# Kernel tuning notes

Hardware: AMD Instinct MI355X
Metric: run time of the kernel (lower is better)

Reference implementation:

```python
import jax, jax.numpy as jnp
import numpy as np

B, N, C, H = 4, 2048, 768, 12
D = C // H  # head_dim = 64

def setup_inputs() -> dict:
    key = jax.random.key(0)
    ks = jax.random.split(key, 6)
    s = 0.02
    return {
        "img_tokens": jax.random.normal(ks[0], (B, N, C), jnp.float32),
        "ln_gamma": jnp.ones((C,), jnp.float32),
        "ln_beta": jnp.zeros((C,), jnp.float32),
        "w_qkv": jax.random.normal(ks[1], (C, 3 * C), jnp.float32) * s,
        "w_out": jax.random.normal(ks[2], (C, C), jnp.float32) * s,
        "b_out": jnp.zeros((C,), jnp.float32),
    }

def reference(img_tokens, ln_gamma, ln_beta, w_qkv, w_out, b_out):
    x = img_tokens
    # LayerNorm over channel dim
    mu = jnp.mean(x, axis=-1, keepdims=True)
    var = jnp.var(x, axis=-1, keepdims=True)
    xn = (x - mu) * jax.lax.rsqrt(var + 1e-5) * ln_gamma + ln_beta
    qkv = xn @ w_qkv                      # [B, N, 3C]
    q, k, v = jnp.split(qkv, 3, axis=-1)
    def heads(t):                          # [B, N, C] -> [B, H, N, D]
        return t.reshape(B, N, H, D).transpose(0, 2, 1, 3)
    q, k, v = heads(q), heads(k), heads(v)
    scale = 1.0 / np.sqrt(D).astype(np.float32)
    scores = jnp.einsum('bhnd,bhmd->bhnm', q, k) * scale  # [B, H, N, N]
    attn = jax.nn.softmax(scores, axis=-1)
    out = jnp.einsum('bhnm,bhmd->bhnd', attn, v)          # [B, H, N, D]
    out = out.transpose(0, 2, 1, 3).reshape(B, N, C)
    out = out @ w_out + b_out
    return out + img_tokens
```

## Files before the change

### kernel.cpp

```cpp
#include <hip/hip_runtime.h>


typedef __bf16 bf16x8 __attribute__((ext_vector_type(8)));
typedef float  f32x4  __attribute__((ext_vector_type(4)));
typedef unsigned int u32x4 __attribute__((ext_vector_type(4)));

#define MFMA16(a,b,c) __builtin_amdgcn_mfma_f32_16x16x32_bf16((a),(b),(c),0,0,0)

__device__ inline f32x4 zero4() { f32x4 z = {0.f,0.f,0.f,0.f}; return z; }

__device__ inline void gll16(const __bf16* g, __bf16* l) {
  __builtin_amdgcn_global_load_lds((const __attribute__((address_space(1))) unsigned int*)g,
                                   (__attribute__((address_space(3))) unsigned int*)l,
                                   16, 0, 0);
}

__device__ inline unsigned cvt_pk_bf16(float lo, float hi) {
  unsigned r;
  asm("v_cvt_pk_bf16_f32 %0, %1, %2" : "=v"(r) : "v"(lo), "v"(hi));
  return r;
}
__device__ inline void permlane32_swap(unsigned &a, unsigned &b) {
  asm("v_permlane32_swap_b32 %0, %1" : "+v"(a), "+v"(b));
}
__device__ inline void permlane16_swap(unsigned &a, unsigned &b) {
  asm("v_permlane16_swap_b32 %0, %1" : "+v"(a), "+v"(b));
}

__global__ __launch_bounds__(256) void ln_kernel(const float* __restrict__ x,
                                                 const float* __restrict__ g,
                                                 const float* __restrict__ bt,
                                                 __bf16* __restrict__ xn) {
  const int row = blockIdx.x;
  const int tid = threadIdx.x;
  const float* xr = x + (size_t)row * 768;
  float v[3]; float s = 0.f, ss = 0.f;
  #pragma unroll
  for (int i = 0; i < 3; ++i) { float f = xr[tid + 256*i]; v[i] = f; s += f; ss += f*f; }
  #pragma unroll
  for (int m = 32; m >= 1; m >>= 1) { s += __shfl_xor(s, m, 64); ss += __shfl_xor(ss, m, 64); }
  __shared__ float red[8];
  const int wave = tid >> 6;
  if ((tid & 63) == 0) { red[wave] = s; red[4 + wave] = ss; }
  __syncthreads();
  s  = red[0] + red[1] + red[2] + red[3];
  ss = red[4] + red[5] + red[6] + red[7];
  const float mu  = s * (1.f/768.f);
  const float var = ss * (1.f/768.f) - mu*mu;
  const float inv = rsqrtf(var + 1e-5f);
  __bf16* xo = xn + (size_t)row * 768;
  #pragma unroll
  for (int i = 0; i < 3; ++i) {
    const int c0 = tid + 256*i;
    xo[c0] = (__bf16)((v[i] - mu) * inv * g[c0] + bt[c0]);
  }
}

__global__ __launch_bounds__(256) void transpose_kernel(const float* __restrict__ in,
                                                        __bf16* __restrict__ out,
                                                        int R, int C) {
  __shared__ float t[32][33];
  const int tx = threadIdx.x & 31, ty = threadIdx.x >> 5;
  const int c0 = blockIdx.x * 32, r0 = blockIdx.y * 32;
  #pragma unroll
  for (int p = 0; p < 4; ++p) t[ty + 8*p][tx] = in[(size_t)(r0 + ty + 8*p) * C + c0 + tx];
  __syncthreads();
  #pragma unroll
  for (int p = 0; p < 4; ++p) out[(size_t)(c0 + ty + 8*p) * R + r0 + tx] = (__bf16)t[tx][ty + 8*p];
}

template<int KDIM>
__device__ inline void gemm_mainloop(const __bf16* __restrict__ A, const __bf16* __restrict__ BT,
                                     int bm, int bn, int wave, int lane,
                                     f32x4 acc[4][4], __bf16* Asm, __bf16* Bsm) {
  const int wm = wave >> 1, wn = wave & 1;
  const int lr = lane & 15, lk = lane >> 4;
  constexpr int NIT = KDIM / 64;
  auto stage = [&](int t) {
    const int k0 = t * 64;
    __bf16* Ad = Asm + (t & 1) * 8192;
    __bf16* Bd = Bsm + (t & 1) * 8192;
    #pragma unroll
    for (int s2 = 0; s2 < 4; ++s2) {
      const int st = wave * 4 + s2;
      const int rb = st >> 1, kh = st & 1;
      gll16(A  + (size_t)(bm + rb*16 + lr) * KDIM + k0 + kh*32 + lk*8, Ad + st*512);
      gll16(BT + (size_t)(bn + rb*16 + lr) * KDIM + k0 + kh*32 + lk*8, Bd + st*512);
    }
  };
  stage(0);
  stage(1);
  for (int t = 0; t < NIT; ++t) {
    if (t + 1 < NIT) asm volatile("s_waitcnt vmcnt(8)" ::: "memory");
    else             asm volatile("s_waitcnt vmcnt(0)" ::: "memory");
    asm volatile("s_barrier" ::: "memory");
    const __bf16* Ab = Asm + (t & 1) * 8192;
    const __bf16* Bb = Bsm + (t & 1) * 8192;
    #pragma unroll
    for (int ks = 0; ks < 2; ++ks) {
      bf16x8 a[4], b[4];
      #pragma unroll
      for (int mt = 0; mt < 4; ++mt) a[mt] = *(const bf16x8*)(Ab + ((wm*4+mt)*2+ks)*512 + lane*8);
      #pragma unroll
      for (int nt = 0; nt < 4; ++nt) b[nt] = *(const bf16x8*)(Bb + ((wn*4+nt)*2+ks)*512 + lane*8);
      __builtin_amdgcn_s_setprio(1);
      #pragma unroll
      for (int mt = 0; mt < 4; ++mt)
        #pragma unroll
        for (int nt = 0; nt < 4; ++nt)
          acc[mt][nt] = MFMA16(a[mt], b[nt], acc[mt][nt]);
      __builtin_amdgcn_s_setprio(0);
    }
    asm volatile("s_barrier" ::: "memory");
    if (t + 2 < NIT) stage(t + 2);
  }
}

__global__ __launch_bounds__(256) void gemm_qkv_kernel(const __bf16* __restrict__ A,
                                                       const __bf16* __restrict__ BT,
                                                       __bf16* __restrict__ q,
                                                       __bf16* __restrict__ k,
                                                       __bf16* __restrict__ vt) {
  __shared__ __align__(16) __bf16 smem[4*8192];
  __bf16* Asm = smem;
  __bf16* Bsm = smem + 2*8192;
  const int lane = threadIdx.x & 63, wave = threadIdx.x >> 6;
  const int bm = blockIdx.y * 128, bn = blockIdx.x * 128;
  f32x4 acc[4][4];
  #pragma unroll
  for (int i = 0; i < 4; ++i)
    #pragma unroll
    for (int j = 0; j < 4; ++j) acc[i][j] = zero4();
  gemm_mainloop<768>(A, BT, bm, bn, wave, lane, acc, Asm, Bsm);
  const int wm = wave >> 1, wn = wave & 1;
  const int quad = lane >> 4, c = lane & 15;
  if (bn < 1536) {
    const float qscale = 0.125f * 1.44269504088896f;
    #pragma unroll
    for (int mt = 0; mt < 4; ++mt)
      #pragma unroll
      for (int nt = 0; nt < 4; ++nt) {
        const int col = bn + wn*64 + nt*16 + c;
        const int which = col >= 768 ? 1 : 0;
        const int within = col - which*768;
        const int h = within >> 6, d = within & 63;
        #pragma unroll
        for (int r = 0; r < 4; ++r) {
          const int row = bm + wm*64 + mt*16 + quad*4 + r;
          const int b = row >> 11, n = row & 2047;
          const float vv = acc[mt][nt][r];
          const size_t idx = ((size_t)(b*12 + h) * 2048 + n) * 64 + d;
          if (which == 0) q[idx] = (__bf16)(vv * qscale);
          else            k[idx] = (__bf16)vv;
        }
      }
  } else {
    __syncthreads();
    #pragma unroll
    for (int mt = 0; mt < 4; ++mt)
      #pragma unroll
      for (int nt = 0; nt < 4; ++nt) {
        const int lcol = wn*64 + nt*16 + c;
        #pragma unroll
        for (int r = 0; r < 4; ++r) {
          const int lrow = wm*64 + mt*16 + quad*4 + r;
          smem[lrow*66 + lcol] = (__bf16)acc[mt][nt][r];
        }
      }
    __syncthreads();
    const int b = bm >> 11, n0 = bm & 2047;
    const int vo = bn - 1536;
    const int n = threadIdx.x & 127;
    const int csel = threadIdx.x >> 7;
    #pragma unroll
    for (int pass = 0; pass < 64; ++pass) {
      const int lc = pass*2 + csel;
      const int gcol = vo + lc;
      const int h = gcol >> 6, d = gcol & 63;
      vt[((size_t)(b*12 + h)*64 + d)*2048 + n0 + n] = smem[n*66 + lc];
    }
  }
}

__global__ __launch_bounds__(256) void gemm_out_kernel(const __bf16* __restrict__ A,
                                                       const __bf16* __restrict__ BT,
                                                       const float* __restrict__ bias,
                                                       const float* __restrict__ resid,
                                                       float* __restrict__ out) {
  __shared__ __align__(16) __bf16 Asm[2*8192];
  __shared__ __align__(16) __bf16 Bsm[2*8192];
  const int lane = threadIdx.x & 63, wave = threadIdx.x >> 6;
  const int bm = blockIdx.y * 128, bn = blockIdx.x * 128;
  f32x4 acc[4][4];
  #pragma unroll
  for (int i = 0; i < 4; ++i)
    #pragma unroll
    for (int j = 0; j < 4; ++j) acc[i][j] = zero4();
  gemm_mainloop<768>(A, BT, bm, bn, wave, lane, acc, Asm, Bsm);
  const int wm = wave >> 1, wn = wave & 1;
  const int quad = lane >> 4, c = lane & 15;
  #pragma unroll
  for (int mt = 0; mt < 4; ++mt)
    #pragma unroll
    for (int nt = 0; nt < 4; ++nt) {
      const int col = bn + wn*64 + nt*16 + c;
      #pragma unroll
      for (int r = 0; r < 4; ++r) {
        const int row = bm + wm*64 + mt*16 + quad*4 + r;
        out[(size_t)row*768 + col] = acc[mt][nt][r] + bias[col] + resid[(size_t)row*768 + col];
      }
    }
}

__global__ __launch_bounds__(512, 6) void attn_kernel(const __bf16* __restrict__ q,
                                                      const __bf16* __restrict__ k,
                                                      const __bf16* __restrict__ vt,
                                                      __bf16* __restrict__ o) {
  const int xcd = blockIdx.x & 7, i = blockIdx.x >> 3;
  const int bh = xcd * 6 + (i >> 4);
  const int qt = i & 15;
  const int lane = threadIdx.x & 63, wave = threadIdx.x >> 6;
  const int c = lane & 15, quad = lane >> 4;
  const int lr = lane & 15, lk = lane >> 4;
  const int q0 = qt*128 + wave*16;

  const __bf16* qb = q  + ((size_t)bh*2048 + q0) * 64;
  const __bf16* kb = k  + (size_t)bh * 2048 * 64;
  const __bf16* vb = vt + (size_t)bh * 64 * 2048;

  __shared__ __align__(16) __bf16 Ksm[2][4096];
  __shared__ __align__(16) __bf16 Vsm[2][4096];

  bf16x8 aq[2];
  aq[0] = *(const bf16x8*)(qb + (size_t)c*64 + quad*8);
  aq[1] = *(const bf16x8*)(qb + (size_t)c*64 + 32 + quad*8);

  float cl = 0.f;
  f32x4 od[4];
  #pragma unroll
  for (int r = 0; r < 4; ++r) od[r] = zero4();

  auto stage = [&](int it) {
    const int kt = it * 64;
    __bf16* Ks = Ksm[it & 1];
    __bf16* Vs = Vsm[it & 1];
    gll16(kb + (size_t)(kt + (wave>>1)*16 + lr) * 64 + (wave&1)*32 + lk*8,  Ks + wave*512);
    gll16(vb + (size_t)((wave>>1)*16 + lr) * 2048 + kt + (wave&1)*32 + lk*8, Vs + wave*512);
  };

  stage(0);
  stage(1);

  for (int it = 0; it < 32; ++it) {
    const __bf16* Ks = Ksm[it & 1];
    const __bf16* Vs = Vsm[it & 1];
    if (it < 31) asm volatile("s_waitcnt vmcnt(2)" ::: "memory");
    else         asm volatile("s_waitcnt vmcnt(0)" ::: "memory");
    asm volatile("s_barrier" ::: "memory");
    #pragma unroll
    for (int ch = 0; ch < 2; ++ch) {
      unsigned pk[2][2];
      #pragma unroll
      for (int t2 = 0; t2 < 2; ++t2) {
        const int t = ch*2 + t2;
        const bf16x8 ka0 = *(const bf16x8*)(Ks + (t*2+0)*512 + lane*8);
        const bf16x8 ka1 = *(const bf16x8*)(Ks + (t*2+1)*512 + lane*8);
        f32x4 z = zero4();
        __builtin_amdgcn_s_setprio(1);
        z = MFMA16(ka0, aq[0], z);
        z = MFMA16(ka1, aq[1], z);
        __builtin_amdgcn_s_setprio(0);
        const float p0 = __builtin_amdgcn_exp2f(z[0]);
        const float p1 = __builtin_amdgcn_exp2f(z[1]);
        const float p2 = __builtin_amdgcn_exp2f(z[2]);
        const float p3 = __builtin_amdgcn_exp2f(z[3]);
        cl += (p0 + p1) + (p2 + p3);
        pk[t2][0] = cvt_pk_bf16(p0, p1);
        pk[t2][1] = cvt_pk_bf16(p2, p3);
      }
      unsigned s0 = pk[0][0], s2 = pk[1][0];
      permlane32_swap(s0, s2);
      permlane16_swap(s0, s2);
      unsigned s1 = pk[0][1], s3 = pk[1][1];
      permlane32_swap(s1, s3);
      permlane16_swap(s1, s3);
      u32x4 w4; w4.x = s0; w4.y = s1; w4.z = s2; w4.w = s3;
      const bf16x8 pa = __builtin_bit_cast(bf16x8, w4);
      __builtin_amdgcn_s_setprio(1);
      #pragma unroll
      for (int dt = 0; dt < 4; ++dt) {
        const bf16x8 bv = *(const bf16x8*)(Vs + (dt*2+ch)*512 + lane*8);
        od[dt] = MFMA16(pa, bv, od[dt]);
      }
      __builtin_amdgcn_s_setprio(0);
    }
    asm volatile("s_barrier" ::: "memory");
    if (it + 2 < 32) stage(it + 2);
  }
  const int b = bh / 12, h = bh % 12;
  float s = cl;
  s += __shfl_xor(s, 16, 64);
  s += __shfl_xor(s, 32, 64);
  float rl[4];
  #pragma unroll
  for (int r = 0; r < 4; ++r) rl[r] = 1.f / __shfl(s, quad*4 + r, 64);
  #pragma unroll
  for (int dt = 0; dt < 4; ++dt)
    #pragma unroll
    for (int r = 0; r < 4; ++r) {
      const int n = q0 + quad*4 + r;
      const int col = h*64 + dt*16 + c;
      o[((size_t)b*2048 + n)*768 + col] = (__bf16)(od[dt][r] * rl[r]);
    }
}

extern "C" void kernel_launch(void* const* d_in, const int* in_sizes, int n_in,
                              void* d_out, int out_size, void* d_ws, size_t ws_size,
                              hipStream_t stream) {
  const float* img   = (const float*)d_in[0];
  const float* gamma = (const float*)d_in[1];
  const float* beta  = (const float*)d_in[2];
  const float* wqkv  = (const float*)d_in[3];
  const float* wout  = (const float*)d_in[4];
  const float* bout  = (const float*)d_in[5];
  float* out = (float*)d_out;

  __bf16* ws = (__bf16*)d_ws;
  size_t off = 0;
  __bf16* xn    = ws + off; off += (size_t)8192*768;
  __bf16* wqkvT = ws + off; off += (size_t)2304*768;
  __bf16* woutT = ws + off; off += (size_t)768*768;
  __bf16* qs    = ws + off; off += (size_t)48*2048*64;
  __bf16* ks    = ws + off; off += (size_t)48*2048*64;
  __bf16* vts   = ws + off; off += (size_t)48*64*2048;
  __bf16* os    = ws + off; off += (size_t)8192*768;

  ln_kernel<<<8192, 256, 0, stream>>>(img, gamma, beta, xn);
  transpose_kernel<<<dim3(72, 24), 256, 0, stream>>>(wqkv, wqkvT, 768, 2304);
  transpose_kernel<<<dim3(24, 24), 256, 0, stream>>>(wout, woutT, 768, 768);
  gemm_qkv_kernel<<<dim3(18, 64), 256, 0, stream>>>(xn, wqkvT, qs, ks, vts);
  attn_kernel<<<768, 512, 0, stream>>>(qs, ks, vts, os);
  gemm_out_kernel<<<dim3(6, 64), 256, 0, stream>>>(os, woutT, bout, img, out);
}
```

Before: 246.9 us.

## Load V directly from global into registers and compute row sums with MFMA

Drops the LDS staging buffer for the transposed V tile. Each wave now loads its V fragments straight from global memory into registers, and only K stays double-buffered through LDS. The softmax denominator is no longer a scalar running sum reduced with shuffles at the end. It is accumulated by an extra MFMA of the probability fragment against a ones vector. This cuts LDS traffic, LDS footprint and the final cross-lane reduction, but all eight waves now read the same V data from global or L2. The explicit vmcnt wait for K now happens only on the first iteration and otherwise relies on compiler-inserted waits.

```diff
diff --git a/kernel.cpp b/kernel.cpp
--- a/kernel.cpp
+++ b/kernel.cpp
@@ -229,36 +229,41 @@
   const __bf16* vb = vt + (size_t)bh * 64 * 2048;
 
   __shared__ __align__(16) __bf16 Ksm[2][4096];
-  __shared__ __align__(16) __bf16 Vsm[2][4096];
 
   bf16x8 aq[2];
   aq[0] = *(const bf16x8*)(qb + (size_t)c*64 + quad*8);
   aq[1] = *(const bf16x8*)(qb + (size_t)c*64 + 32 + quad*8);
 
-  float cl = 0.f;
+  const __bf16 one = (__bf16)1.0f;
+  bf16x8 vones;
+  #pragma unroll
+  for (int j = 0; j < 8; ++j) vones[j] = one;
+
   f32x4 od[4];
+  f32x4 clacc = zero4();
   #pragma unroll
   for (int r = 0; r < 4; ++r) od[r] = zero4();
 
-  auto stage = [&](int it) {
+  auto stageK = [&](int it) {
     const int kt = it * 64;
-    __bf16* Ks = Ksm[it & 1];
-    __bf16* Vs = Vsm[it & 1];
-    gll16(kb + (size_t)(kt + (wave>>1)*16 + lr) * 64 + (wave&1)*32 + lk*8,  Ks + wave*512);
-    gll16(vb + (size_t)((wave>>1)*16 + lr) * 2048 + kt + (wave&1)*32 + lk*8, Vs + wave*512);
+    gll16(kb + (size_t)(kt + (wave>>1)*16 + lr) * 64 + (wave&1)*32 + lk*8,
+          Ksm[it & 1] + wave*512);
   };
 
-  stage(0);
-  stage(1);
+  stageK(0);
+  stageK(1);
 
   for (int it = 0; it < 32; ++it) {
     const __bf16* Ks = Ksm[it & 1];
-    const __bf16* Vs = Vsm[it & 1];
-    if (it < 31) asm volatile("s_waitcnt vmcnt(2)" ::: "memory");
-    else         asm volatile("s_waitcnt vmcnt(0)" ::: "memory");
+    const int kt = it * 64;
+    if (it == 0) asm volatile("s_waitcnt vmcnt(0)" ::: "memory");
     asm volatile("s_barrier" ::: "memory");
     #pragma unroll
     for (int ch = 0; ch < 2; ++ch) {
+      bf16x8 vr[4];
+      #pragma unroll
+      for (int dt = 0; dt < 4; ++dt)
+        vr[dt] = *(const bf16x8*)(vb + (size_t)(dt*16 + lr) * 2048 + kt + ch*32 + lk*8);
       unsigned pk[2][2];
       #pragma unroll
       for (int t2 = 0; t2 < 2; ++t2) {
@@ -274,7 +279,6 @@
         const float p1 = __builtin_amdgcn_exp2f(z[1]);
         const float p2 = __builtin_amdgcn_exp2f(z[2]);
         const float p3 = __builtin_amdgcn_exp2f(z[3]);
-        cl += (p0 + p1) + (p2 + p3);
         pk[t2][0] = cvt_pk_bf16(p0, p1);
         pk[t2][1] = cvt_pk_bf16(p2, p3);
       }
@@ -288,22 +292,18 @@
       const bf16x8 pa = __builtin_bit_cast(bf16x8, w4);
       __builtin_amdgcn_s_setprio(1);
       #pragma unroll
-      for (int dt = 0; dt < 4; ++dt) {
-        const bf16x8 bv = *(const bf16x8*)(Vs + (dt*2+ch)*512 + lane*8);
-        od[dt] = MFMA16(pa, bv, od[dt]);
-      }
+      for (int dt = 0; dt < 4; ++dt)
+        od[dt] = MFMA16(pa, vr[dt], od[dt]);
+      clacc = MFMA16(pa, vones, clacc);
       __builtin_amdgcn_s_setprio(0);
     }
     asm volatile("s_barrier" ::: "memory");
-    if (it + 2 < 32) stage(it + 2);
+    if (it + 2 < 32) stageK(it + 2);
   }
   const int b = bh / 12, h = bh % 12;
-  float s = cl;
-  s += __shfl_xor(s, 16, 64);
-  s += __shfl_xor(s, 32, 64);
   float rl[4];
   #pragma unroll
-  for (int r = 0; r < 4; ++r) rl[r] = 1.f / __shfl(s, quad*4 + r, 64);
+  for (int r = 0; r < 4; ++r) rl[r] = 1.f / clacc[r];
   #pragma unroll
   for (int dt = 0; dt < 4; ++dt)
     #pragma unroll
```

Result: slower. 377.8 us (+53.0%).
